# Kernel tuning notes

Measured on AMD Instinct MI355X. Metric: run time of the kernel, lower is better.

The kernel has to match this reference:

```python
import jax, jax.numpy as jnp
import numpy as np

BITS = 4
GROUP = 128
K = 8192      # infeatures
N = 28672     # outfeatures
M = 32        # batch of tokens (decode-style small M)


def setup_inputs() -> dict:
    key = jax.random.key(0)
    k1, k2, k3, k4 = jax.random.split(key, 4)
    A = jax.random.normal(k1, (M, K), dtype=jnp.float16)
    # packed uint4 weights: two nibbles per byte, stored as int32 holding 0..255
    qweight = jax.random.randint(k2, (N, K // 2), 0, 256, dtype=jnp.int32)
    scales = (jax.random.normal(k3, (N, K // GROUP)) * 0.01).astype(jnp.float16)
    zeros = (jax.random.uniform(k4, (N, K // GROUP)) * 15.0).astype(jnp.float16)
    bias = jnp.zeros((N,), dtype=jnp.float16)
    return {"A": A, "qweight": qweight, "scales": scales, "zeros": zeros, "bias": bias}


def _dequantize(qweight, scales, zeros):
    # unpack two uint4 values per byte, low nibble first (matches unpack_qzeros order)
    low = qweight & 15
    high = (qweight >> 4) & 15
    w_int = jnp.stack([low, high], axis=-1).reshape(qweight.shape[0], -1)  # (N, K)
    w = w_int.astype(jnp.float16)
    n, k = w.shape
    wg = w.reshape(n, k // GROUP, GROUP)
    # 'original' zeros type: (w - zero) * scale, per (out_channel, group)
    wd = (wg - zeros[:, :, None]) * scales[:, :, None]
    return wd.reshape(n, k)  # (N, K) fp16


def reference(A, qweight, scales, zeros, bias):
    W = _dequantize(qweight, scales, zeros)          # (N, K)
    C = jnp.einsum("mk,nk->mn", A, W) + bias[None, :]  # (M, N)
    return C.astype(A.dtype)
```

## Files before the change

### kernel.cpp

```cpp
#include <hip/hip_runtime.h>

#define KK 8192
#define NN 28672
#define MM 32
#define NBLK 16
#define NBLOCKS (NN / NBLK)
#define WTILES 16

typedef __bf16 bf16;
typedef bf16  bf16x8 __attribute__((ext_vector_type(8)));
typedef float floatx4 __attribute__((ext_vector_type(4)));

__global__ __launch_bounds__(256) void aconv_kernel(const float* __restrict__ A,
                                                    bf16* __restrict__ Ab) {
  const int i = (blockIdx.x * 256 + threadIdx.x) * 8;
  const float4 fa = *(const float4*)(A + i);
  const float4 fb = *(const float4*)(A + i + 4);
  bf16x8 o;
  o[0] = (bf16)fa.x; o[1] = (bf16)fa.y; o[2] = (bf16)fa.z; o[3] = (bf16)fa.w;
  o[4] = (bf16)fb.x; o[5] = (bf16)fb.y; o[6] = (bf16)fb.z; o[7] = (bf16)fb.w;
  *(bf16x8*)(Ab + i) = o;
}

__global__ __launch_bounds__(256, 4) void qgemm_kernel(
    const bf16* __restrict__ Ab, const int* __restrict__ qw,
    const float* __restrict__ scales, const float* __restrict__ zeros,
    const float* __restrict__ bias, float* __restrict__ out) {
  __shared__ float red[3][64][8];

  const int tid = threadIdx.x;
  const int wv  = tid >> 6;
  const int l   = tid & 63;
  const int lr  = l & 15;
  const int lg  = l >> 4;
  const int n0  = blockIdx.x * NBLK;

  const int kb_e = wv * 2048;
  const int kb_i = wv * 1024;
  const int gb   = wv * WTILES;

  const float4* sp = (const float4*)(scales + (n0 + lr) * 64 + gb);
  const float4* zp = (const float4*)(zeros  + (n0 + lr) * 64 + gb);

  floatx4 acc[2];
  acc[0] = (floatx4){0.f, 0.f, 0.f, 0.f};
  acc[1] = (floatx4){0.f, 0.f, 0.f, 0.f};

#pragma unroll
  for (int q = 0; q < 4; ++q) {
    const float4 sv = sp[q];
    const float4 zv = zp[q];
#pragma unroll
    for (int u = 0; u < 4; ++u) {
      const int t = q * 4 + u;
      const float c1 = (u == 0) ? sv.x : (u == 1) ? sv.y : (u == 2) ? sv.z : sv.w;
      const float zz = (u == 0) ? zv.x : (u == 1) ? zv.y : (u == 2) ? zv.z : zv.w;
      const float c0 = -(128.f + zz) * c1;

#pragma unroll
      for (int s = 0; s < 4; ++s) {
        const uint4 v = *(const uint4*)(qw + (n0 + lr) * 4096 + kb_i + t * 64 + (s * 4 + lg) * 4);
        bf16x8 bfr;
#pragma unroll
        for (int i = 0; i < 4; ++i) {
          const unsigned qd = ((const unsigned*)&v)[i];
          const float lo = __builtin_bit_cast(float, 0x43000000u | ((qd & 0x0Fu) << 16));
          const float hi = __builtin_bit_cast(float, 0x43000000u | ((qd & 0xF0u) << 12));
          bfr[2 * i]     = (bf16)__builtin_fmaf(lo, c1, c0);
          bfr[2 * i + 1] = (bf16)__builtin_fmaf(hi, c1, c0);
        }
#pragma unroll
        for (int mt = 0; mt < 2; ++mt) {
          const bf16x8 af = *(const bf16x8*)(Ab + (mt * 16 + lr) * KK + kb_e + t * 128 + s * 32 + lg * 8);
          acc[mt] = __builtin_amdgcn_mfma_f32_16x16x32_bf16(af, bfr, acc[mt], 0, 0, 0);
        }
      }
    }
  }

  if (wv > 0) {
#pragma unroll
    for (int mt = 0; mt < 2; ++mt)
#pragma unroll
      for (int r = 0; r < 4; ++r)
        red[wv - 1][l][mt * 4 + r] = acc[mt][r];
  }
  __syncthreads();
  if (wv == 0) {
#pragma unroll
    for (int mt = 0; mt < 2; ++mt)
#pragma unroll
      for (int r = 0; r < 4; ++r) {
        float v = acc[mt][r];
#pragma unroll
        for (int w2 = 0; w2 < 3; ++w2) v += red[w2][l][mt * 4 + r];
        const int m = mt * 16 + lg * 4 + r;
        const int n = n0 + lr;
        out[m * NN + n] = v + bias[n];
      }
  }
}

extern "C" void kernel_launch(void* const* d_in, const int* in_sizes, int n_in,
                              void* d_out, int out_size, void* d_ws, size_t ws_size,
                              hipStream_t stream) {
  const float* A    = (const float*)d_in[0];
  const int*   qw   = (const int*)d_in[1];
  const float* sc   = (const float*)d_in[2];
  const float* zr   = (const float*)d_in[3];
  const float* bias = (const float*)d_in[4];
  float*       out  = (float*)d_out;
  bf16*        Ab   = (bf16*)d_ws;

  aconv_kernel<<<dim3(MM * KK / (256 * 8)), dim3(256), 0, stream>>>(A, Ab);
  qgemm_kernel<<<dim3(NBLOCKS), dim3(256), 0, stream>>>(Ab, qw, sc, zr, bias, out);
}
```

Baseline: 698.5 us.

## Switch to fp16 MFMA with packed half2 dequant and double-buffered weight loads

```diff
diff --git a/kernel.cpp b/kernel.cpp
--- a/kernel.cpp
+++ b/kernel.cpp
@@ -7,23 +7,39 @@
 #define NBLOCKS (NN / NBLK)
 #define WTILES 16
 
-typedef __bf16 bf16;
-typedef bf16  bf16x8 __attribute__((ext_vector_type(8)));
+typedef _Float16 h1;
+typedef h1    h2 __attribute__((ext_vector_type(2)));
+typedef h1    h8 __attribute__((ext_vector_type(8)));
 typedef float floatx4 __attribute__((ext_vector_type(4)));
 
 __global__ __launch_bounds__(256) void aconv_kernel(const float* __restrict__ A,
-                                                    bf16* __restrict__ Ab) {
+                                                    h1* __restrict__ Ah) {
   const int i = (blockIdx.x * 256 + threadIdx.x) * 8;
   const float4 fa = *(const float4*)(A + i);
   const float4 fb = *(const float4*)(A + i + 4);
-  bf16x8 o;
-  o[0] = (bf16)fa.x; o[1] = (bf16)fa.y; o[2] = (bf16)fa.z; o[3] = (bf16)fa.w;
-  o[4] = (bf16)fb.x; o[5] = (bf16)fb.y; o[6] = (bf16)fb.z; o[7] = (bf16)fb.w;
-  *(bf16x8*)(Ab + i) = o;
+  h8 o;
+  o[0] = (h1)fa.x; o[1] = (h1)fa.y; o[2] = (h1)fa.z; o[3] = (h1)fa.w;
+  o[4] = (h1)fb.x; o[5] = (h1)fb.y; o[6] = (h1)fb.z; o[7] = (h1)fb.w;
+  *(h8*)(Ah + i) = o;
+}
+
+__device__ __forceinline__ h8 dequant8(const uint4 v, const h2 spk, const h2 mzspk) {
+  h8 w;
+#pragma unroll
+  for (int i = 0; i < 4; ++i) {
+    const unsigned q = ((const unsigned*)&v)[i];
+    const unsigned t = q | (q << 12);
+    const unsigned p = (t & 0x000F000Fu) | 0x64006400u;
+    const h2 e = __builtin_bit_cast(h2, p) + (h2){(h1)(-1024.f), (h1)(-1024.f)};
+    const h2 wv = e * spk + mzspk;
+    w[2 * i]     = wv.x;
+    w[2 * i + 1] = wv.y;
+  }
+  return w;
 }
 
 __global__ __launch_bounds__(256, 4) void qgemm_kernel(
-    const bf16* __restrict__ Ab, const int* __restrict__ qw,
+    const h1* __restrict__ Ah, const int* __restrict__ qw,
     const float* __restrict__ scales, const float* __restrict__ zeros,
     const float* __restrict__ bias, float* __restrict__ out) {
   __shared__ float red[3][64][8];
@@ -39,6 +55,10 @@
   const int kb_i = wv * 1024;
   const int gb   = wv * WTILES;
 
+  const int* qbase = qw + (n0 + lr) * 4096 + kb_i + lg * 4;
+  const h1* abase0 = Ah + lr * KK + kb_e + lg * 8;
+  const h1* abase1 = abase0 + 16 * KK;
+
   const float4* sp = (const float4*)(scales + (n0 + lr) * 64 + gb);
   const float4* zp = (const float4*)(zeros  + (n0 + lr) * 64 + gb);
 
@@ -46,33 +66,36 @@
   acc[0] = (floatx4){0.f, 0.f, 0.f, 0.f};
   acc[1] = (floatx4){0.f, 0.f, 0.f, 0.f};
 
+  uint4 b[2][4];
 #pragma unroll
-  for (int q = 0; q < 4; ++q) {
-    const float4 sv = sp[q];
-    const float4 zv = zp[q];
+  for (int s = 0; s < 4; ++s) b[0][s] = *(const uint4*)(qbase + s * 16);
+
+#pragma unroll
+  for (int q4 = 0; q4 < 4; ++q4) {
+    const float4 sv = sp[q4];
+    const float4 zv = zp[q4];
 #pragma unroll
     for (int u = 0; u < 4; ++u) {
-      const int t = q * 4 + u;
-      const float c1 = (u == 0) ? sv.x : (u == 1) ? sv.y : (u == 2) ? sv.z : sv.w;
-      const float zz = (u == 0) ? zv.x : (u == 1) ? zv.y : (u == 2) ? zv.z : zv.w;
-      const float c0 = -(128.f + zz) * c1;
+      const int t = q4 * 4 + u;
+      if (t + 1 < WTILES) {
+#pragma unroll
+        for (int s = 0; s < 4; ++s)
+          b[(t + 1) & 1][s] = *(const uint4*)(qbase + (t + 1) * 64 + s * 16);
+      }
+      const float sf = (u == 0) ? sv.x : (u == 1) ? sv.y : (u == 2) ? sv.z : sv.w;
+      const float zf = (u == 0) ? zv.x : (u == 1) ? zv.y : (u == 2) ? zv.z : zv.w;
+      const h2 spk   = {(h1)sf, (h1)sf};
+      const float mz = -zf * sf;
+      const h2 mzspk = {(h1)mz, (h1)mz};
 
 #pragma unroll
       for (int s = 0; s < 4; ++s) {
-        const uint4 v = *(const uint4*)(qw + (n0 + lr) * 4096 + kb_i + t * 64 + (s * 4 + lg) * 4);
-        bf16x8 bfr;
-#pragma unroll
-        for (int i = 0; i < 4; ++i) {
-          const unsigned qd = ((const unsigned*)&v)[i];
-          const float lo = __builtin_bit_cast(float, 0x43000000u | ((qd & 0x0Fu) << 16));
-          const float hi = __builtin_bit_cast(float, 0x43000000u | ((qd & 0xF0u) << 12));
-          bfr[2 * i]     = (bf16)__builtin_fmaf(lo, c1, c0);
-          bfr[2 * i + 1] = (bf16)__builtin_fmaf(hi, c1, c0);
-        }
+        const h8 bfr = dequant8(b[t & 1][s], spk, mzspk);
 #pragma unroll
         for (int mt = 0; mt < 2; ++mt) {
-          const bf16x8 af = *(const bf16x8*)(Ab + (mt * 16 + lr) * KK + kb_e + t * 128 + s * 32 + lg * 8);
-          acc[mt] = __builtin_amdgcn_mfma_f32_16x16x32_bf16(af, bfr, acc[mt], 0, 0, 0);
+          const h1* ap = (mt == 0 ? abase0 : abase1) + t * 128 + s * 32;
+          const h8 af = *(const h8*)(ap);
+          acc[mt] = __builtin_amdgcn_mfma_f32_16x16x32_f16(af, bfr, acc[mt], 0, 0, 0);
         }
       }
     }
@@ -110,8 +133,8 @@
   const float* zr   = (const float*)d_in[3];
   const float* bias = (const float*)d_in[4];
   float*       out  = (float*)d_out;
-  bf16*        Ab   = (bf16*)d_ws;
+  h1*          Ah   = (h1*)d_ws;
 
-  aconv_kernel<<<dim3(MM * KK / (256 * 8)), dim3(256), 0, stream>>>(A, Ab);
-  qgemm_kernel<<<dim3(NBLOCKS), dim3(256), 0, stream>>>(Ab, qw, sc, zr, bias, out);
+  aconv_kernel<<<dim3(MM * KK / (256 * 8)), dim3(256), 0, stream>>>(A, Ah);
+  qgemm_kernel<<<dim3(NBLOCKS), dim3(256), 0, stream>>>(Ah, qw, sc, zr, bias, out);
 }
```

After: 692.7 us. About the same (-0.8%).
